# Performance work log

Hardware: AMD Instinct MI355X
Metric: run time of the kernel (lower is better)

Reference implementation:

```python
import jax, jax.numpy as jnp
import numpy as np

NUM_USERS = 30000
NUM_ITEMS = 30000
N = NUM_USERS + NUM_ITEMS          # total graph nodes (users + items)
E = 800000                          # number of edges
EMBED_K = 64
INTENTS = 4
D = EMBED_K // INTENTS              # per-intent channel chunk
N_LAYERS = 1
ROUTING_ITERS = 2


def setup_inputs() -> dict:
    key = jax.random.key(0)
    k1, k2, k3, k4 = jax.random.split(key, 4)
    Gu = jax.random.normal(k1, (NUM_USERS, EMBED_K), jnp.float32) * 0.1
    Gi = jax.random.normal(k2, (NUM_ITEMS, EMBED_K), jnp.float32) * 0.1
    # head list: guarantee every node appears at least once as a head so that
    # D = 1/sqrt(row_degree) is finite (real CF graphs have no isolated rows)
    edge_h = jnp.concatenate([jnp.arange(N, dtype=jnp.int64),
                              jax.random.randint(k3, (E - N,), 0, N, dtype=jnp.int64)])
    edge_t = jax.random.randint(k4, (E,), 0, N, dtype=jnp.int64)
    return {"Gu": Gu, "Gi": Gi, "edge_h": edge_h, "edge_t": edge_t}


def _l2norm(x, eps=1e-12):
    # matches torch.nn.functional.normalize(dim=-1)
    return x / jnp.sqrt(jnp.maximum(jnp.sum(x * x, axis=-1, keepdims=True), eps))


def reference(Gu, Gi, edge_h, edge_t):
    ego = jnp.concatenate([Gu, Gi], axis=0)            # [N, K]
    all_emb = [ego]
    # routing attention logits per intent per edge (initialized to ones)
    A_values = jnp.ones((INTENTS, E), dtype=Gu.dtype)
    for _ in range(N_LAYERS):
        # split embed dim into INTENTS contiguous chunks -> [I, N, D]
        X = ego.reshape(N, INTENTS, D).transpose(1, 0, 2)
        Z = X
        for _t in range(ROUTING_ITERS):
            # softmax over intents per edge (pick=False path; p_train is always False)
            scores = jax.nn.softmax(A_values, axis=0)                    # [I, E]
            # per-intent row degrees (sparse.sum over dim=1 indexes rows = heads)
            deg = jnp.zeros((INTENTS, N), scores.dtype).at[:, edge_h].add(scores)
            d_col = 1.0 / jnp.sqrt(deg)                                  # [I, N]
            # D_col @ X, A @ (.), D_col @ (.)  -- note original applies D_col twice (as written)
            Y = d_col[..., None] * X                                     # [I, N, D]
            msg = scores[..., None] * Y[:, edge_t, :]                    # [I, E, D]
            Z = jnp.zeros((INTENTS, N, D), X.dtype).at[:, edge_h, :].add(msg)
            Z = d_col[..., None] * Z                                     # [I, N, D]
            # attention update: normalize(head) . tanh(normalize(tail))
            head = _l2norm(Z[:, edge_h, :])                              # [I, E, D]
            tail = _l2norm(X[:, edge_t, :])                              # [I, E, D]
            A_values = A_values + jnp.sum(head * jnp.tanh(tail), axis=-1)
        # concat intent chunks back along channel dim
        ego = Z.transpose(1, 0, 2).reshape(N, EMBED_K)
        all_emb.append(ego)
    out = jnp.mean(jnp.stack(all_emb, axis=1), axis=1)   # [N, K]
    return out[:NUM_USERS], out[NUM_USERS:]
```

## Files before the change

kernel.cpp:

```cpp
#include <hip/hip_runtime.h>
#include <hip/hip_fp16.h>


#define NUSERS 30000
#define NN     60000
#define EE     800000
#define SCAN_B ((NN + 255) / 256)
#define EV_B   ((EE / 4 + 255) / 256)
#define NW1_B  ((NN + 1 + 3) / 4)
#define N8_B   (NN / 8)

__device__ __forceinline__ float getX(const float* __restrict__ Gu,
                                      const float* __restrict__ Gi,
                                      int n, int c) {
    return (n < NUSERS) ? Gu[n * 64 + c] : Gi[(n - NUSERS) * 64 + c];
}

__device__ __forceinline__ int clampN(int n) {
    return ((unsigned)n < (unsigned)NN) ? n : 0;
}

__device__ __forceinline__ __half2 bch2(float f) {
    return __builtin_bit_cast(__half2, f);
}

__global__ void count_prep(const int* __restrict__ eh, int* __restrict__ deg0,
                           int* __restrict__ rank,
                           const float* __restrict__ Gu, const float* __restrict__ Gi,
                           __half* __restrict__ Xh, __half* __restrict__ Ttab) {
    if (blockIdx.x < EV_B) {
        int e4 = (blockIdx.x * 256 + threadIdx.x) * 4;
        if (e4 >= EE) return;
        int4 h = *(const int4*)(eh + e4);
        int4 r;
        r.x = atomicAdd(&deg0[clampN(h.x)], 1);
        r.y = atomicAdd(&deg0[clampN(h.y)], 1);
        r.z = atomicAdd(&deg0[clampN(h.z)], 1);
        r.w = atomicAdd(&deg0[clampN(h.w)], 1);
        *(int4*)(rank + e4) = r;
    } else {
        int n = (blockIdx.x - EV_B) * 4 + (threadIdx.x >> 6);
        if (n > NN) return;
        int lane = threadIdx.x & 63;
        float x = (n < NN) ? getX(Gu, Gi, n, lane) : 0.f;
        float sx = x * x;
        #pragma unroll
        for (int m = 1; m < 16; m <<= 1) sx += __shfl_xor(sx, m, 64);
        float invx = rsqrtf(fmaxf(sx, 1e-12f));
        size_t a = (size_t)n * 64 + lane;
        Xh[a]   = __float2half(x);
        Ttab[a] = __float2half(tanhf(x * invx));
    }
}

__global__ void scan_local(const int* __restrict__ deg0, int* __restrict__ offsets,
                           int* __restrict__ bsum, float* __restrict__ d0a) {
    int gid = blockIdx.x * 256 + threadIdx.x;
    int lane = threadIdx.x & 63, w = threadIdx.x >> 6;
    int vdeg = (gid < NN) ? deg0[gid] : 0;
    if (gid < NN) d0a[gid] = rsqrtf(fmaxf(0.25f * (float)vdeg, 1e-30f));
    if (gid == NN) d0a[NN] = 0.f;
    int x = vdeg;
    #pragma unroll
    for (int d = 1; d < 64; d <<= 1) {
        int y = __shfl_up(x, d, 64);
        if (lane >= d) x += y;
    }
    __shared__ int wsum[4];
    if (lane == 63) wsum[w] = x;
    __syncthreads();
    int wpre = 0;
    #pragma unroll
    for (int j = 0; j < 4; ++j) wpre += (j < w) ? wsum[j] : 0;
    int incl = x + wpre;
    if (gid < NN) offsets[gid] = incl - vdeg;
    if (threadIdx.x == 255) bsum[blockIdx.x] = incl;
}

__global__ void scan_add2(int* __restrict__ offsets, const int* __restrict__ bsum) {
    int tid = threadIdx.x, lane = tid & 63, w = tid >> 6;
    int vv = (tid < SCAN_B) ? bsum[tid] : 0;
    int x = vv;
    #pragma unroll
    for (int d = 1; d < 64; d <<= 1) {
        int y = __shfl_up(x, d, 64);
        if (lane >= d) x += y;
    }
    __shared__ int wsum[4];
    __shared__ int bpre;
    if (lane == 63) wsum[w] = x;
    __syncthreads();
    int wpre = 0;
    #pragma unroll
    for (int j = 0; j < 4; ++j) wpre += (j < w) ? wsum[j] : 0;
    if (tid == blockIdx.x) bpre = x + wpre - vv;
    __syncthreads();
    int gid = blockIdx.x * 256 + tid;
    if (gid < NN) offsets[gid] += bpre;
    if (gid == 0) offsets[NN] = EE;
}

__global__ void scatter(const int* __restrict__ eh, const int* __restrict__ et,
                        const int* __restrict__ rank, const int* __restrict__ offsets,
                        int* __restrict__ csr_tail) {
    int e4 = (blockIdx.x * 256 + threadIdx.x) * 4;
    if (e4 >= EE) return;
    int4 h = *(const int4*)(eh + e4);
    int4 t = *(const int4*)(et + e4);
    int4 r = *(const int4*)(rank + e4);
    int s0 = offsets[clampN(h.x)] + r.x;
    if ((unsigned)s0 < EE) csr_tail[s0] = clampN(t.x);
    int s1 = offsets[clampN(h.y)] + r.y;
    if ((unsigned)s1 < EE) csr_tail[s1] = clampN(t.y);
    int s2 = offsets[clampN(h.z)] + r.z;
    if ((unsigned)s2 < EE) csr_tail[s2] = clampN(t.z);
    int s3 = offsets[clampN(h.w)] + r.w;
    if ((unsigned)s3 < EE) csr_tail[s3] = clampN(t.w);
}

__global__ void zat(const int* __restrict__ offsets, const int* __restrict__ csr_tail,
                    const __half* __restrict__ Xh, const float* __restrict__ d0a,
                    const __half* __restrict__ Ttab,
                    __half* __restrict__ s4, float* __restrict__ dcol1) {
    __shared__ __half zn[8][72];
    __shared__ float ssum[8][4];
    __shared__ int soff[9];
    int tid = threadIdx.x;
    int n0 = blockIdx.x * 8;
    if (tid < 9) soff[tid] = offsets[n0 + tid];
    if (tid >= 32 && tid < 64) ssum[(tid - 32) >> 2][tid & 3] = 0.f;
    __syncthreads();

    {
        int g = tid >> 5, cc = tid & 31;
        int s0 = soff[g], s1 = soff[g + 1];
        float accx = 0.f, accy = 0.f;
        for (int base = s0; base < s1; base += 4) {
            #pragma unroll
            for (int u = 0; u < 4; ++u) {
                int kk = base + u;
                bool act = kk < s1;
                int kc = act ? kk : s0;
                int t = act ? csr_tail[kc] : NN;
                float d0v = d0a[t];
                __half2 y = *(const __half2*)(Xh + (size_t)t * 64 + cc * 2);
                float2 yf = __half22float2(y);
                accx = fmaf(d0v, yf.x, accx);
                accy = fmaf(d0v, yf.y, accy);
            }
        }
        float ss = accx * accx + accy * accy;
        ss += __shfl_xor(ss, 1, 64);
        ss += __shfl_xor(ss, 2, 64);
        ss += __shfl_xor(ss, 4, 64);
        float inv = rsqrtf(fmaxf(ss, 1e-12f));
        *(__half2*)&zn[g][cc * 2] = __floats2half2_rn(accx * inv, accy * inv);
    }
    __syncthreads();

    int e0 = soff[0], e1 = soff[8];
    for (int k = e0 + tid; k < e1; k += 256) {
        int hl = 0;
        #pragma unroll
        for (int j = 1; j < 8; ++j) hl += (k >= soff[j]) ? 1 : 0;
        int t = csr_tail[k];
        const float4* tp = (const float4*)(Ttab + (size_t)t * 64);
        float dot[4];
        #pragma unroll
        for (int i = 0; i < 4; ++i) {
            float4 za = *(const float4*)&zn[hl][i * 16];
            float4 zb = *(const float4*)&zn[hl][i * 16 + 8];
            float4 ta = tp[2 * i], tb = tp[2 * i + 1];
            __half2 acc = __floats2half2_rn(0.f, 0.f);
            acc = __hfma2(bch2(za.x), bch2(ta.x), acc);
            acc = __hfma2(bch2(za.y), bch2(ta.y), acc);
            acc = __hfma2(bch2(za.z), bch2(ta.z), acc);
            acc = __hfma2(bch2(za.w), bch2(ta.w), acc);
            acc = __hfma2(bch2(zb.x), bch2(tb.x), acc);
            acc = __hfma2(bch2(zb.y), bch2(tb.y), acc);
            acc = __hfma2(bch2(zb.z), bch2(tb.z), acc);
            acc = __hfma2(bch2(zb.w), bch2(tb.w), acc);
            float2 f = __half22float2(acc);
            dot[i] = f.x + f.y;
        }
        float mx = fmaxf(fmaxf(dot[0], dot[1]), fmaxf(dot[2], dot[3]));
        float q0 = __expf(dot[0] - mx), q1 = __expf(dot[1] - mx);
        float q2 = __expf(dot[2] - mx), q3 = __expf(dot[3] - mx);
        float inv = 1.f / (q0 + q1 + q2 + q3);
        q0 *= inv; q1 *= inv; q2 *= inv; q3 *= inv;
        __half2 o01 = __floats2half2_rn(q0, q1);
        __half2 o23 = __floats2half2_rn(q2, q3);
        int2 st;
        st.x = __builtin_bit_cast(int, o01);
        st.y = __builtin_bit_cast(int, o23);
        *(int2*)(s4 + (size_t)k * 4) = st;
        atomicAdd(&ssum[hl][0], q0);
        atomicAdd(&ssum[hl][1], q1);
        atomicAdd(&ssum[hl][2], q2);
        atomicAdd(&ssum[hl][3], q3);
    }
    __syncthreads();

    if (tid < 32) {
        int nn = n0 + (tid >> 2);
        dcol1[nn * 4 + (tid & 3)] = rsqrtf(fmaxf(ssum[tid >> 2][tid & 3], 1e-30f));
    }
}

__global__ void outk(const int* __restrict__ offsets, const int* __restrict__ csr_tail,
                     const __half* __restrict__ Xh, const __half* __restrict__ s4,
                     const float* __restrict__ dcol1,
                     const float* __restrict__ Gu, const float* __restrict__ Gi,
                     float* __restrict__ out) {
    int tid = threadIdx.x;
    int n = blockIdx.x * 8 + (tid >> 5);
    if (n >= NN) return;
    int cc = tid & 31;
    int i = cc >> 3;
    int s0 = offsets[n], s1 = offsets[n + 1];
    float accx = 0.f, accy = 0.f;
    for (int base = s0; base < s1; base += 4) {
        #pragma unroll
        for (int u = 0; u < 4; ++u) {
            int kk = base + u;
            bool act = kk < s1;
            int kc = act ? kk : s0;
            int t = csr_tail[kc];
            int2 raw = *(const int2*)(s4 + (size_t)kc * 4);
            int word = (cc & 16) ? raw.y : raw.x;
            unsigned short us = (unsigned short)(word >> ((cc & 8) ? 16 : 0));
            float s = act ? __half2float(__builtin_bit_cast(__half, us)) : 0.f;
            float w = s * dcol1[t * 4 + i];
            __half2 y = *(const __half2*)(Xh + (size_t)t * 64 + cc * 2);
            float2 yf = __half22float2(y);
            accx = fmaf(w, yf.x, accx);
            accy = fmaf(w, yf.y, accy);
        }
    }
    float d = dcol1[n * 4 + i];
    int ch = cc * 2;
    const float* xr = (n < NUSERS) ? (Gu + (size_t)n * 64 + ch)
                                   : (Gi + (size_t)(n - NUSERS) * 64 + ch);
    float2 x2 = *(const float2*)xr;
    float2 o;
    o.x = 0.5f * (x2.x + d * accx);
    o.y = 0.5f * (x2.y + d * accy);
    *(float2*)(out + (size_t)n * 64 + ch) = o;
}


extern "C" void kernel_launch(void* const* d_in, const int* in_sizes, int n_in,
                              void* d_out, int out_size, void* d_ws, size_t ws_size,
                              hipStream_t stream) {
    const float* Gu = (const float*)d_in[0];
    const float* Gi = (const float*)d_in[1];
    const int* eh = (const int*)d_in[2];
    const int* et = (const int*)d_in[3];
    float* out = (float*)d_out;

    char* p = (char*)d_ws;
    __half* s4       = (__half*)p;     p += (size_t)EE * 4 * 2;
    int*    csr_tail = (int*)p;        p += (size_t)EE * 4;
    int*    rank     = (int*)p;        p += (size_t)EE * 4;
    int*    offsets  = (int*)p;        p += ((size_t)(NN + 1) * 4 + 15) / 16 * 16;
    int*    deg0     = (int*)p;        p += (size_t)NN * 4;
    int*    bsum     = (int*)p;        p += ((size_t)SCAN_B * 4 + 15) / 16 * 16;
    float*  dcol1    = (float*)p;      p += (size_t)NN * 4 * 4;
    float*  d0a      = (float*)p;      p += ((size_t)(NN + 1) * 4 + 15) / 16 * 16;
    __half* Xh       = (__half*)p;     p += (size_t)(NN + 1) * 64 * 2;
    __half* Ttab     = (__half*)p;

    hipMemsetAsync(deg0, 0, NN * sizeof(int), stream);
    count_prep<<<EV_B + NW1_B, 256, 0, stream>>>(eh, deg0, rank, Gu, Gi, Xh, Ttab);
    scan_local<<<SCAN_B, 256, 0, stream>>>(deg0, offsets, bsum, d0a);
    scan_add2<<<SCAN_B, 256, 0, stream>>>(offsets, bsum);

    scatter<<<EV_B, 256, 0, stream>>>(eh, et, rank, offsets, csr_tail);

    zat<<<N8_B, 256, 0, stream>>>(offsets, csr_tail, Xh, d0a, Ttab, s4, dcol1);

    outk<<<N8_B, 256, 0, stream>>>(offsets, csr_tail, Xh, s4, dcol1, Gu, Gi, out);
}
```

Measured before the change: 234.9 us.

## Split per-intent tables and pin each intent to an XCD pair

Reorganizes node tables into intent-major planar layouts (Yq, Tq) with the first-iteration degree scaling folded into Yq, and maps blocks so that each intent is handled by a fixed pair of XCDs. The aim is to shrink each XCD's gathered working set so it stays in its local L2. The cost is that the per-edge softmax can no longer run inside zat, which now writes raw dots to a new float buffer. A separate combine kernel then does the softmax and degree sums, adding a launch and extra global traffic. Table prep moves into the scan-add kernel.

```diff
diff --git a/kernel.cpp b/kernel.cpp
--- a/kernel.cpp
+++ b/kernel.cpp
@@ -4,11 +4,13 @@
 
 #define NUSERS 30000
 #define NN     60000
+#define NNP    (NN + 1)
 #define EE     800000
 #define SCAN_B ((NN + 255) / 256)
 #define EV_B   ((EE / 4 + 255) / 256)
 #define NW1_B  ((NN + 1 + 3) / 4)
-#define N8_B   (NN / 8)
+#define GPI    ((NN + 31) / 32)
+#define PIN_B  ((((GPI + 1) / 2) * 8))
 
 __device__ __forceinline__ float getX(const float* __restrict__ Gu,
                                       const float* __restrict__ Gi,
@@ -24,33 +26,18 @@
     return __builtin_bit_cast(__half2, f);
 }
 
-__global__ void count_prep(const int* __restrict__ eh, int* __restrict__ deg0,
-                           int* __restrict__ rank,
-                           const float* __restrict__ Gu, const float* __restrict__ Gi,
-                           __half* __restrict__ Xh, __half* __restrict__ Ttab) {
-    if (blockIdx.x < EV_B) {
-        int e4 = (blockIdx.x * 256 + threadIdx.x) * 4;
-        if (e4 >= EE) return;
-        int4 h = *(const int4*)(eh + e4);
-        int4 r;
-        r.x = atomicAdd(&deg0[clampN(h.x)], 1);
-        r.y = atomicAdd(&deg0[clampN(h.y)], 1);
-        r.z = atomicAdd(&deg0[clampN(h.z)], 1);
-        r.w = atomicAdd(&deg0[clampN(h.w)], 1);
-        *(int4*)(rank + e4) = r;
-    } else {
-        int n = (blockIdx.x - EV_B) * 4 + (threadIdx.x >> 6);
-        if (n > NN) return;
-        int lane = threadIdx.x & 63;
-        float x = (n < NN) ? getX(Gu, Gi, n, lane) : 0.f;
-        float sx = x * x;
-        #pragma unroll
-        for (int m = 1; m < 16; m <<= 1) sx += __shfl_xor(sx, m, 64);
-        float invx = rsqrtf(fmaxf(sx, 1e-12f));
-        size_t a = (size_t)n * 64 + lane;
-        Xh[a]   = __float2half(x);
-        Ttab[a] = __float2half(tanhf(x * invx));
-    }
+
+__global__ void edge_count(const int* __restrict__ eh, int* __restrict__ deg0,
+                           int* __restrict__ rank) {
+    int e4 = (blockIdx.x * blockDim.x + threadIdx.x) * 4;
+    if (e4 >= EE) return;
+    int4 h = *(const int4*)(eh + e4);
+    int4 r;
+    r.x = atomicAdd(&deg0[clampN(h.x)], 1);
+    r.y = atomicAdd(&deg0[clampN(h.y)], 1);
+    r.z = atomicAdd(&deg0[clampN(h.z)], 1);
+    r.w = atomicAdd(&deg0[clampN(h.w)], 1);
+    *(int4*)(rank + e4) = r;
 }
 
 __global__ void scan_local(const int* __restrict__ deg0, int* __restrict__ offsets,
@@ -77,27 +64,46 @@
     if (threadIdx.x == 255) bsum[blockIdx.x] = incl;
 }
 
-__global__ void scan_add2(int* __restrict__ offsets, const int* __restrict__ bsum) {
-    int tid = threadIdx.x, lane = tid & 63, w = tid >> 6;
-    int vv = (tid < SCAN_B) ? bsum[tid] : 0;
-    int x = vv;
-    #pragma unroll
-    for (int d = 1; d < 64; d <<= 1) {
-        int y = __shfl_up(x, d, 64);
-        if (lane >= d) x += y;
-    }
-    __shared__ int wsum[4];
-    __shared__ int bpre;
-    if (lane == 63) wsum[w] = x;
-    __syncthreads();
-    int wpre = 0;
-    #pragma unroll
-    for (int j = 0; j < 4; ++j) wpre += (j < w) ? wsum[j] : 0;
-    if (tid == blockIdx.x) bpre = x + wpre - vv;
-    __syncthreads();
-    int gid = blockIdx.x * 256 + tid;
-    if (gid < NN) offsets[gid] += bpre;
-    if (gid == 0) offsets[NN] = EE;
+__global__ void scanadd2_prep(int* __restrict__ offsets, const int* __restrict__ bsum,
+                              const float* __restrict__ d0a,
+                              const float* __restrict__ Gu, const float* __restrict__ Gi,
+                              __half* __restrict__ Yq, __half* __restrict__ Tq) {
+    if (blockIdx.x < SCAN_B) {
+        int tid = threadIdx.x, lane = tid & 63, w = tid >> 6;
+        int vv = (tid < SCAN_B) ? bsum[tid] : 0;
+        int x = vv;
+        #pragma unroll
+        for (int d = 1; d < 64; d <<= 1) {
+            int y = __shfl_up(x, d, 64);
+            if (lane >= d) x += y;
+        }
+        __shared__ int wsum[4];
+        __shared__ int bpre;
+        if (lane == 63) wsum[w] = x;
+        __syncthreads();
+        int wpre = 0;
+        #pragma unroll
+        for (int j = 0; j < 4; ++j) wpre += (j < w) ? wsum[j] : 0;
+        if (tid == blockIdx.x) bpre = x + wpre - vv;
+        __syncthreads();
+        int gid = blockIdx.x * 256 + tid;
+        if (gid < NN) offsets[gid] += bpre;
+        if (gid == 0) offsets[NN] = EE;
+    } else {
+        int n = (blockIdx.x - SCAN_B) * 4 + (threadIdx.x >> 6);
+        if (n > NN) return;
+        int lane = threadIdx.x & 63;
+        int i = lane >> 4, cl = lane & 15;
+        float x = (n < NN) ? getX(Gu, Gi, n, lane) : 0.f;
+        float sx = x * x;
+        #pragma unroll
+        for (int m = 1; m < 16; m <<= 1) sx += __shfl_xor(sx, m, 64);
+        float invx = rsqrtf(fmaxf(sx, 1e-12f));
+        float d0v = d0a[n];
+        size_t a = ((size_t)i * NNP + n) * 16 + cl;
+        Yq[a] = __float2half(d0v * x);
+        Tq[a] = __float2half(tanhf(x * invx));
+    }
 }
 
 __global__ void scatter(const int* __restrict__ eh, const int* __restrict__ et,
@@ -119,21 +125,23 @@
 }
 
 __global__ void zat(const int* __restrict__ offsets, const int* __restrict__ csr_tail,
-                    const __half* __restrict__ Xh, const float* __restrict__ d0a,
-                    const __half* __restrict__ Ttab,
-                    __half* __restrict__ s4, float* __restrict__ dcol1) {
-    __shared__ __half zn[8][72];
-    __shared__ float ssum[8][4];
-    __shared__ int soff[9];
-    int tid = threadIdx.x;
-    int n0 = blockIdx.x * 8;
-    if (tid < 9) soff[tid] = offsets[n0 + tid];
-    if (tid >= 32 && tid < 64) ssum[(tid - 32) >> 2][tid & 3] = 0.f;
+                    const __half* __restrict__ Yq, const __half* __restrict__ Tq,
+                    float* __restrict__ dotq) {
+    __shared__ __half zn[32][24];
+    __shared__ int soff[33];
+    int b = blockIdx.x, tid = threadIdx.x;
+    int xcd = b & 7;
+    int i = xcd >> 1;
+    int g = (b >> 3) * 2 + (xcd & 1);
+    if (g >= GPI) return;
+    int n0 = g * 32;
+    if (tid < 33) soff[tid] = offsets[n0 + tid];
     __syncthreads();
 
     {
-        int g = tid >> 5, cc = tid & 31;
-        int s0 = soff[g], s1 = soff[g + 1];
+        int g8 = tid >> 3, cl = tid & 7;
+        int s0 = soff[g8], s1 = soff[g8 + 1];
+        const __half* Yi = Yq + (size_t)i * NNP * 16;
         float accx = 0.f, accy = 0.f;
         for (int base = s0; base < s1; base += 4) {
             #pragma unroll
@@ -142,11 +150,9 @@
                 bool act = kk < s1;
                 int kc = act ? kk : s0;
                 int t = act ? csr_tail[kc] : NN;
-                float d0v = d0a[t];
-                __half2 y = *(const __half2*)(Xh + (size_t)t * 64 + cc * 2);
+                __half2 y = *(const __half2*)(Yi + (size_t)t * 16 + cl * 2);
                 float2 yf = __half22float2(y);
-                accx = fmaf(d0v, yf.x, accx);
-                accy = fmaf(d0v, yf.y, accy);
+                accx += yf.x; accy += yf.y;
             }
         }
         float ss = accx * accx + accy * accy;
@@ -154,70 +160,92 @@
         ss += __shfl_xor(ss, 2, 64);
         ss += __shfl_xor(ss, 4, 64);
         float inv = rsqrtf(fmaxf(ss, 1e-12f));
-        *(__half2*)&zn[g][cc * 2] = __floats2half2_rn(accx * inv, accy * inv);
+        *(__half2*)&zn[g8][cl * 2] = __floats2half2_rn(accx * inv, accy * inv);
     }
     __syncthreads();
 
-    int e0 = soff[0], e1 = soff[8];
+    int e0 = soff[0], e1 = soff[32];
+    const __half* Ti = Tq + (size_t)i * NNP * 16;
     for (int k = e0 + tid; k < e1; k += 256) {
         int hl = 0;
         #pragma unroll
-        for (int j = 1; j < 8; ++j) hl += (k >= soff[j]) ? 1 : 0;
+        for (int step = 16; step >= 1; step >>= 1)
+            if (soff[hl + step] <= k) hl += step;
         int t = csr_tail[k];
-        const float4* tp = (const float4*)(Ttab + (size_t)t * 64);
-        float dot[4];
-        #pragma unroll
-        for (int i = 0; i < 4; ++i) {
-            float4 za = *(const float4*)&zn[hl][i * 16];
-            float4 zb = *(const float4*)&zn[hl][i * 16 + 8];
-            float4 ta = tp[2 * i], tb = tp[2 * i + 1];
-            __half2 acc = __floats2half2_rn(0.f, 0.f);
-            acc = __hfma2(bch2(za.x), bch2(ta.x), acc);
-            acc = __hfma2(bch2(za.y), bch2(ta.y), acc);
-            acc = __hfma2(bch2(za.z), bch2(ta.z), acc);
-            acc = __hfma2(bch2(za.w), bch2(ta.w), acc);
-            acc = __hfma2(bch2(zb.x), bch2(tb.x), acc);
-            acc = __hfma2(bch2(zb.y), bch2(tb.y), acc);
-            acc = __hfma2(bch2(zb.z), bch2(tb.z), acc);
-            acc = __hfma2(bch2(zb.w), bch2(tb.w), acc);
-            float2 f = __half22float2(acc);
-            dot[i] = f.x + f.y;
-        }
-        float mx = fmaxf(fmaxf(dot[0], dot[1]), fmaxf(dot[2], dot[3]));
-        float q0 = __expf(dot[0] - mx), q1 = __expf(dot[1] - mx);
-        float q2 = __expf(dot[2] - mx), q3 = __expf(dot[3] - mx);
-        float inv = 1.f / (q0 + q1 + q2 + q3);
-        q0 *= inv; q1 *= inv; q2 *= inv; q3 *= inv;
-        __half2 o01 = __floats2half2_rn(q0, q1);
-        __half2 o23 = __floats2half2_rn(q2, q3);
-        int2 st;
-        st.x = __builtin_bit_cast(int, o01);
-        st.y = __builtin_bit_cast(int, o23);
-        *(int2*)(s4 + (size_t)k * 4) = st;
-        atomicAdd(&ssum[hl][0], q0);
-        atomicAdd(&ssum[hl][1], q1);
-        atomicAdd(&ssum[hl][2], q2);
-        atomicAdd(&ssum[hl][3], q3);
-    }
-    __syncthreads();
-
-    if (tid < 32) {
-        int nn = n0 + (tid >> 2);
-        dcol1[nn * 4 + (tid & 3)] = rsqrtf(fmaxf(ssum[tid >> 2][tid & 3], 1e-30f));
+        float4 ta = *(const float4*)(Ti + (size_t)t * 16);
+        float4 tb = *(const float4*)(Ti + (size_t)t * 16 + 8);
+        float4 za = *(const float4*)&zn[hl][0];
+        float4 zb = *(const float4*)&zn[hl][8];
+        __half2 acc = __floats2half2_rn(0.f, 0.f);
+        acc = __hfma2(bch2(za.x), bch2(ta.x), acc);
+        acc = __hfma2(bch2(za.y), bch2(ta.y), acc);
+        acc = __hfma2(bch2(za.z), bch2(ta.z), acc);
+        acc = __hfma2(bch2(za.w), bch2(ta.w), acc);
+        acc = __hfma2(bch2(zb.x), bch2(tb.x), acc);
+        acc = __hfma2(bch2(zb.y), bch2(tb.y), acc);
+        acc = __hfma2(bch2(zb.z), bch2(tb.z), acc);
+        acc = __hfma2(bch2(zb.w), bch2(tb.w), acc);
+        float2 f = __half22float2(acc);
+        dotq[(size_t)i * EE + k] = f.x + f.y;
+    }
+}
+
+__global__ void combine(const int* __restrict__ offsets, const float* __restrict__ dotq,
+                        const float* __restrict__ d0a,
+                        __half* __restrict__ sq, float* __restrict__ d1q,
+                        float* __restrict__ d1rd0q) {
+    int n = blockIdx.x * 4 + (threadIdx.x >> 6);
+    if (n >= NN) return;
+    int lane = threadIdx.x & 63;
+    int s0 = offsets[n], s1 = offsets[n + 1];
+    float sum0 = 0.f, sum1 = 0.f, sum2 = 0.f, sum3 = 0.f;
+    for (int k = s0 + lane; k < s1; k += 64) {
+        float v0 = dotq[k];
+        float v1 = dotq[EE + k];
+        float v2 = dotq[2 * EE + k];
+        float v3 = dotq[3 * EE + k];
+        float mx = fmaxf(fmaxf(v0, v1), fmaxf(v2, v3));
+        float e0 = __expf(v0 - mx), e1 = __expf(v1 - mx);
+        float e2 = __expf(v2 - mx), e3 = __expf(v3 - mx);
+        float inv = 1.f / (e0 + e1 + e2 + e3);
+        e0 *= inv; e1 *= inv; e2 *= inv; e3 *= inv;
+        sq[k]          = __float2half(e0);
+        sq[EE + k]     = __float2half(e1);
+        sq[2 * EE + k] = __float2half(e2);
+        sq[3 * EE + k] = __float2half(e3);
+        sum0 += e0; sum1 += e1; sum2 += e2; sum3 += e3;
+    }
+    #pragma unroll
+    for (int m = 1; m < 64; m <<= 1) {
+        sum0 += __shfl_xor(sum0, m, 64);
+        sum1 += __shfl_xor(sum1, m, 64);
+        sum2 += __shfl_xor(sum2, m, 64);
+        sum3 += __shfl_xor(sum3, m, 64);
+    }
+    if (lane < 4) {
+        float ds = (lane == 0) ? sum0 : (lane == 1) ? sum1 : (lane == 2) ? sum2 : sum3;
+        float d1 = rsqrtf(fmaxf(ds, 1e-30f));
+        d1q[(size_t)lane * NNP + n] = d1;
+        d1rd0q[(size_t)lane * NNP + n] = d1 / d0a[n];
     }
 }
 
 __global__ void outk(const int* __restrict__ offsets, const int* __restrict__ csr_tail,
-                     const __half* __restrict__ Xh, const __half* __restrict__ s4,
-                     const float* __restrict__ dcol1,
+                     const __half* __restrict__ Yq, const __half* __restrict__ sq,
+                     const float* __restrict__ d1q, const float* __restrict__ d1rd0q,
                      const float* __restrict__ Gu, const float* __restrict__ Gi,
                      float* __restrict__ out) {
-    int tid = threadIdx.x;
-    int n = blockIdx.x * 8 + (tid >> 5);
-    if (n >= NN) return;
-    int cc = tid & 31;
-    int i = cc >> 3;
+    int b = blockIdx.x, tid = threadIdx.x;
+    int xcd = b & 7;
+    int i = xcd >> 1;
+    int g = (b >> 3) * 2 + (xcd & 1);
+    if (g >= GPI) return;
+    int n = g * 32 + (tid >> 3);
+    int cl = tid & 7;
     int s0 = offsets[n], s1 = offsets[n + 1];
+    const __half* Yi = Yq + (size_t)i * NNP * 16;
+    const __half* si = sq + (size_t)i * EE;
+    const float* w1 = d1rd0q + (size_t)i * NNP;
     float accx = 0.f, accy = 0.f;
     for (int base = s0; base < s1; base += 4) {
         #pragma unroll
@@ -226,19 +254,16 @@
             bool act = kk < s1;
             int kc = act ? kk : s0;
             int t = csr_tail[kc];
-            int2 raw = *(const int2*)(s4 + (size_t)kc * 4);
-            int word = (cc & 16) ? raw.y : raw.x;
-            unsigned short us = (unsigned short)(word >> ((cc & 8) ? 16 : 0));
-            float s = act ? __half2float(__builtin_bit_cast(__half, us)) : 0.f;
-            float w = s * dcol1[t * 4 + i];
-            __half2 y = *(const __half2*)(Xh + (size_t)t * 64 + cc * 2);
+            float s = act ? __half2float(si[kc]) : 0.f;
+            float w = s * w1[t];
+            __half2 y = *(const __half2*)(Yi + (size_t)t * 16 + cl * 2);
             float2 yf = __half22float2(y);
             accx = fmaf(w, yf.x, accx);
             accy = fmaf(w, yf.y, accy);
         }
     }
-    float d = dcol1[n * 4 + i];
-    int ch = cc * 2;
+    float d = d1q[(size_t)i * NNP + n];
+    int ch = i * 16 + cl * 2;
     const float* xr = (n < NUSERS) ? (Gu + (size_t)n * 64 + ch)
                                    : (Gi + (size_t)(n - NUSERS) * 64 + ch);
     float2 x2 = *(const float2*)xr;
@@ -259,25 +284,30 @@
     float* out = (float*)d_out;
 
     char* p = (char*)d_ws;
-    __half* s4       = (__half*)p;     p += (size_t)EE * 4 * 2;
+    float*  dotq     = (float*)p;      p += (size_t)EE * 4 * 4;
+    __half* sq       = (__half*)p;     p += (size_t)EE * 4 * 2;
     int*    csr_tail = (int*)p;        p += (size_t)EE * 4;
     int*    rank     = (int*)p;        p += (size_t)EE * 4;
-    int*    offsets  = (int*)p;        p += ((size_t)(NN + 1) * 4 + 15) / 16 * 16;
+    int*    offsets  = (int*)p;        p += ((size_t)NNP * 4 + 15) / 16 * 16;
     int*    deg0     = (int*)p;        p += (size_t)NN * 4;
     int*    bsum     = (int*)p;        p += ((size_t)SCAN_B * 4 + 15) / 16 * 16;
-    float*  dcol1    = (float*)p;      p += (size_t)NN * 4 * 4;
-    float*  d0a      = (float*)p;      p += ((size_t)(NN + 1) * 4 + 15) / 16 * 16;
-    __half* Xh       = (__half*)p;     p += (size_t)(NN + 1) * 64 * 2;
-    __half* Ttab     = (__half*)p;
+    float*  d0a      = (float*)p;      p += ((size_t)NNP * 4 + 15) / 16 * 16;
+    float*  d1q      = (float*)p;      p += (size_t)4 * NNP * 4;
+    float*  d1rd0q   = (float*)p;      p += (size_t)4 * NNP * 4;
+    __half* Yq       = (__half*)p;     p += (size_t)4 * NNP * 16 * 2;
+    __half* Tq       = (__half*)p;
 
     hipMemsetAsync(deg0, 0, NN * sizeof(int), stream);
-    count_prep<<<EV_B + NW1_B, 256, 0, stream>>>(eh, deg0, rank, Gu, Gi, Xh, Ttab);
+    edge_count<<<EV_B, 256, 0, stream>>>(eh, deg0, rank);
     scan_local<<<SCAN_B, 256, 0, stream>>>(deg0, offsets, bsum, d0a);
-    scan_add2<<<SCAN_B, 256, 0, stream>>>(offsets, bsum);
-
+    scanadd2_prep<<<SCAN_B + NW1_B, 256, 0, stream>>>(offsets, bsum, d0a,
+                                                      Gu, Gi, Yq, Tq);
     scatter<<<EV_B, 256, 0, stream>>>(eh, et, rank, offsets, csr_tail);
 
-    zat<<<N8_B, 256, 0, stream>>>(offsets, csr_tail, Xh, d0a, Ttab, s4, dcol1);
-
-    outk<<<N8_B, 256, 0, stream>>>(offsets, csr_tail, Xh, s4, dcol1, Gu, Gi, out);
-}
+    zat<<<PIN_B, 256, 0, stream>>>(offsets, csr_tail, Yq, Tq, dotq);
+
+    combine<<<(NN + 3) / 4, 256, 0, stream>>>(offsets, dotq, d0a, sq, d1q, d1rd0q);
+
+    outk<<<PIN_B, 256, 0, stream>>>(offsets, csr_tail, Yq, sq, d1q, d1rd0q,
+                                    Gu, Gi, out);
+}
```

After: 258.2 us. +9.9%, slower.
